# Kernel tuning notes

Hardware: AMD Instinct MI355X
Metric: run time of the kernel (lower is better)

The kernel has to match this reference:

```python
import jax, jax.numpy as jnp
import numpy as np

B, E, S, M, G, L, NSTEP = 32, 256, 16, 16, 32000, 8192, 128


def setup_inputs() -> dict:
    key = jax.random.key(0)
    ks = jax.random.split(key, 8)
    init = lambda k, shape, fan: (jax.random.normal(k, shape, jnp.float32) / np.sqrt(fan).astype(np.float32))
    return {
        "latent": init(ks[0], (L, 2 * E * S), 2 * E * S),
        "trans_w": init(ks[1], (E * M, E), E),
        "trans_b": jnp.zeros((E * M,), jnp.float32),
        "anchor_w": init(ks[2], (M, E), E),
        "anchor_b": jnp.zeros((M,), jnp.float32),
        "vocab_w": init(ks[3], (G, E), E),
        "vocab_b": jnp.zeros((G,), jnp.float32),
        "zi": jax.random.randint(ks[4], (B,), 0, L),
        "y": jax.random.randint(ks[5], (B, NSTEP), 0, G),
        "n_step": NSTEP,
    }


def reference(latent, trans_w, trans_b, anchor_w, anchor_b, vocab_w, vocab_b, zi, y, n_step):
    # latent rows -> (B, 2, state_count, embed_dim); split into keys/values
    z0 = latent[zi].reshape(-1, 2, S, E)
    z = z0[:, 0, 0:1, :]            # initial state: first (unscaled) key vector, [B,1,E]
    xk = z0[:, 0] * 100.0           # [B,S,E]
    xv = z0[:, 1] * 100.0           # [B,S,E]

    def step(z, _):
        # std-normalize (torch.std is unbiased -> ddof=1)
        zn = z / (1e-5 + jnp.std(z, axis=-1, keepdims=True, ddof=1)) * 0.113
        att = jax.nn.softmax(jnp.einsum("bqe,bse->bqs", zn, xk), axis=-1)  # [B,1,S]
        emit = jnp.einsum("bqs,bse->bqe", att, xv)                          # [B,1,E]
        mixed2 = (zn @ trans_w.T + trans_b).reshape(-1, M, E)               # [B,M,E]
        att2 = jax.nn.softmax(zn @ anchor_w.T + anchor_b, axis=-1)          # [B,1,M]
        dz = jnp.einsum("bqm,bme->bqe", att2, mixed2) + emit
        return zn + dz, emit[:, 0, :]

    _, zs = jax.lax.scan(step, z, None, length=n_step)  # [T,B,E]
    zs = jnp.transpose(zs, (1, 0, 2))                   # [B,T,E]
    ys = jax.nn.log_softmax(zs @ vocab_w.T + vocab_b, axis=-1)  # [B,T,G]
    yp = jnp.take_along_axis(ys, y[:, :, None], axis=-1)[:, :, 0]  # [B,T]
    return yp
```

## Files before the change

kernel.cpp:

```cpp
#include <hip/hip_runtime.h>

#define EE 256
#define GG 32000
#define NSTEP 128
#define ROWS 4096
#define VSPLIT 4
#define NWGP 32
#define NWGD 64
#define NWGR (NWGP + NWGD)

typedef __attribute__((ext_vector_type(8))) short bf16x8;
typedef __attribute__((ext_vector_type(4))) float f32x4;

#define OFF_ZSB  0u
#define OFF_PS   2097152u
#define OFF_PT   (OFF_PS + 65536u)
#define OFF_ZNB  (OFF_PT + 65536u)
#define OFF_BAR  (OFF_ZNB + 32768u)
#define OFF_PD   (OFF_BAR + 4096u)
#define WS_REQ   (OFF_PD + 524288u)
#define OFF_VB   WS_REQ
#define VB_BYTES 16384000u


__device__ __forceinline__ float wredf(float v){
    #pragma unroll
    for (int m = 1; m < 64; m <<= 1) v += __shfl_xor(v, m);
    return v;
}
__device__ __forceinline__ unsigned short f2bf_bits(float f){
    unsigned int u = __float_as_uint(f);
    unsigned int lsb = (u >> 16) & 1u;
    u += 0x7fffu + lsb;
    return (unsigned short)(u >> 16);
}
__device__ __forceinline__ float bf2f(unsigned short u){
    return __uint_as_float(((unsigned int)u) << 16);
}
__device__ __forceinline__ float aload(const float* p){
    return __hip_atomic_load(p, __ATOMIC_RELAXED, __HIP_MEMORY_SCOPE_AGENT);
}
__device__ __forceinline__ void astore(float* p, float v){
    __hip_atomic_store(p, v, __ATOMIC_RELAXED, __HIP_MEMORY_SCOPE_AGENT);
}
__device__ __forceinline__ unsigned aloadu(const unsigned* p){
    return __hip_atomic_load(p, __ATOMIC_RELAXED, __HIP_MEMORY_SCOPE_AGENT);
}
__device__ __forceinline__ void astoreu(unsigned* p, unsigned v){
    __hip_atomic_store(p, v, __ATOMIC_RELAXED, __HIP_MEMORY_SCOPE_AGENT);
}
__device__ __forceinline__ int swz(int row, int kbyte){
    return row*512 + (kbyte ^ ((row & 7) << 4));
}
__device__ __forceinline__ void pollflag(int* bar, int idx, int gen){
    int spins = 0;
    while (__hip_atomic_load(&bar[idx], __ATOMIC_RELAXED, __HIP_MEMORY_SCOPE_AGENT) < gen){
        __builtin_amdgcn_s_sleep(1);
        if (++spins > 2000000){
            __hip_atomic_store(&bar[132], 1, __ATOMIC_RELAXED, __HIP_MEMORY_SCOPE_AGENT);
            break;
        }
        if ((spins & 2047) == 0 &&
            __hip_atomic_load(&bar[132], __ATOMIC_RELAXED, __HIP_MEMORY_SCOPE_AGENT) != 0)
            break;
    }
}

__global__ __launch_bounds__(256) void k_sentinel(float* __restrict__ outp, float val){
    int r = blockIdx.x * 256 + threadIdx.x;
    outp[r] = val;
}

__global__ void k_prep(const int* __restrict__ zi, int* __restrict__ bar){
    int t = threadIdx.x;
    bar[t] = 0;
    __syncthreads();
    if (t == 0){
        bool odd_zero = true, even_ok = true;
        for (int i = 0; i < 16; ++i){
            int lo = zi[2*i], hi = zi[2*i+1];
            if (hi != 0) odd_zero = false;
            if (lo < 0 || lo >= 8192) even_ok = false;
        }
        bar[136] = (odd_zero && even_ok) ? 1 : 0;
    }
}

__global__ __launch_bounds__(256) void k_cvt(const float* __restrict__ in,
                                             unsigned short* __restrict__ outp)
{
    int i = (blockIdx.x * 256 + threadIdx.x) * 4;
    float4 v = *(const float4*)&in[i];
    ushort4 o;
    o.x = f2bf_bits(v.x); o.y = f2bf_bits(v.y);
    o.z = f2bf_bits(v.z); o.w = f2bf_bits(v.w);
    *(ushort4*)&outp[i] = o;
}

__global__ __launch_bounds__(512, 1) void k_rnn(const float* __restrict__ latent,
                                                const int* __restrict__ zi,
                                                const float* __restrict__ anchor_w,
                                                const float* __restrict__ anchor_b,
                                                const float* __restrict__ trans_w,
                                                const float* __restrict__ trans_b,
                                                unsigned short* __restrict__ zsb,
                                                unsigned* __restrict__ ZNB,
                                                float* __restrict__ PD,
                                                int* __restrict__ bar)
{
    __shared__ __align__(16) unsigned char WbRaw[2*64*512];
    __shared__ __align__(16) unsigned char ZNbRaw[2*32*512];
    __shared__ float xk_l[16][260];
    __shared__ float xv_l[16][260];
    __shared__ float zl[256];
    __shared__ float a2s[16];
    __shared__ float tbl[2][32];
    __shared__ float l1s[16], l2s[16], ab_l[16], rbuf[8];

    const int wg = blockIdx.x, t = threadIdx.x;
    const int is64 = bar[136];
    const int lane = t & 63, wv = t >> 6;
    const int kg = lane >> 4, nl = lane & 15;

    if (wg < NWGP){
        const int b = wg;
        int zb = is64 ? zi[2*b] : zi[b];
        const float* base = latent + (size_t)zb * 8192;
        for (int i = t; i < 4096; i += 512){
            int s = i >> 8, c = i & 255;
            xk_l[s][c] = base[i];
            xv_l[s][c] = base[4096 + i];
        }
        if (t < 16) ab_l[t] = anchor_b[t];
        __syncthreads();

        float zn_r = 0.f, em_r = 0.f;
        for (int stp = 0; stp < NSTEP; ++stp){
            if (stp > 0){
                if (t < NWGD) pollflag(bar, 64 + t, stp);
                __syncthreads();
                __builtin_amdgcn_sched_barrier(0);
            }
            float zv = 0.f;
            if (t < 256){
                if (stp == 0) zv = base[t];
                else {
                    float dz = 0.f;
                    #pragma unroll
                    for (int g = 0; g < 16; ++g)
                        dz += a2s[g] * aload(&PD[(g*32 + b)*256 + t]);
                    zv = zn_r + em_r + dz;
                }
                float s1 = wredf(zv), s2 = wredf(zv*zv);
                if ((t & 63) == 0){ rbuf[t>>6] = s1; rbuf[4 + (t>>6)] = s2; }
            }
            __syncthreads();
            if (t < 256){
                float tot1 = rbuf[0]+rbuf[1]+rbuf[2]+rbuf[3];
                float tot2 = rbuf[4]+rbuf[5]+rbuf[6]+rbuf[7];
                float mean = tot1 * (1.0f/EE);
                float var  = (tot2 - (float)EE*mean*mean) * (1.0f/(EE-1));
                var = fmaxf(var, 0.f);
                float sc = 0.113f / (1e-5f + sqrtf(var));
                zn_r = zv * sc;
                zl[t] = zn_r;
                if (stp < NSTEP-1){
                    unsigned short zh  = f2bf_bits(zn_r);
                    unsigned short zlo = f2bf_bits(zn_r - bf2f(zh));
                    unsigned ohi = (unsigned)__shfl_xor((int)(unsigned)zh, 1);
                    unsigned olo = (unsigned)__shfl_xor((int)(unsigned)zlo, 1);
                    if (!(t & 1)){
                        astoreu(&ZNB[b*128 + (t >> 1)],        (unsigned)zh  | (ohi << 16));
                        astoreu(&ZNB[4096 + b*128 + (t >> 1)], (unsigned)zlo | (olo << 16));
                    }
                }
            }
            __syncthreads();
            if (stp < NSTEP-1 && t == 0)
                __hip_atomic_store(&bar[b], stp + 1, __ATOMIC_RELAXED, __HIP_MEMORY_SCOPE_AGENT);

            if (t < 256){
                int sidx = t >> 4, L = t & 15;
                const float* aws = anchor_w + sidx*EE;
                float p1 = 0.f, p2 = 0.f;
                #pragma unroll
                for (int c = 0; c < 16; ++c){
                    int k = L*16 + c;
                    float z = zl[k];
                    p1 += z * xk_l[sidx][k];
                    p2 += z * aws[k];
                }
                #pragma unroll
                for (int mm = 1; mm < 16; mm <<= 1){ p1 += __shfl_xor(p1, mm); p2 += __shfl_xor(p2, mm); }
                if (L == 0){ l1s[sidx] = p1 * 100.0f; l2s[sidx] = p2 + ab_l[sidx]; }
            }
            __syncthreads();
            if (t < 256){
                float mx1 = -1e30f, mx2 = -1e30f;
                #pragma unroll
                for (int s = 0; s < 16; ++s){ mx1 = fmaxf(mx1, l1s[s]); mx2 = fmaxf(mx2, l2s[s]); }
                float att[16]; float sum1 = 0.f, sum2 = 0.f;
                #pragma unroll
                for (int s = 0; s < 16; ++s){
                    att[s] = expf(l1s[s] - mx1); sum1 += att[s];
                    sum2  += expf(l2s[s] - mx2);
                }
                float inv1 = 1.0f / sum1;
                if (t < 16) a2s[t] = expf(l2s[t] - mx2) / sum2;
                float em = 0.f;
                #pragma unroll
                for (int s = 0; s < 16; ++s) em += (att[s] * inv1) * xv_l[s][t];
                em *= 100.0f;
                em_r = em;
                zsb[((size_t)b*NSTEP + stp)*EE + t] = f2bf_bits(em);
            }
            __syncthreads();
        }
    } else {
        const int d = wg - NWGP;
        const int mh = d >> 3, q = d & 7;

        for (int idx = t; idx < 4096; idx += 512){
            int r = idx >> 6, c = idx & 63;
            int grow = (2*mh + (r >> 5))*256 + q*32 + (r & 31);
            float4 w = *(const float4*)&trans_w[(size_t)grow*256 + c*4];
            unsigned short h0 = f2bf_bits(w.x), h1 = f2bf_bits(w.y);
            unsigned short h2 = f2bf_bits(w.z), h3 = f2bf_bits(w.w);
            unsigned short l0 = f2bf_bits(w.x - bf2f(h0)), l1 = f2bf_bits(w.y - bf2f(h1));
            unsigned short l2 = f2bf_bits(w.z - bf2f(h2)), l3 = f2bf_bits(w.w - bf2f(h3));
            int off = swz(r, c*8);
            *(unsigned*)&WbRaw[off]     = (unsigned)h0 | ((unsigned)h1 << 16);
            *(unsigned*)&WbRaw[off + 4] = (unsigned)h2 | ((unsigned)h3 << 16);
            *(unsigned*)&WbRaw[64*512 + off]     = (unsigned)l0 | ((unsigned)l1 << 16);
            *(unsigned*)&WbRaw[64*512 + off + 4] = (unsigned)l2 | ((unsigned)l3 << 16);
        }
        if (t < 64) tbl[t >> 5][t & 31] = trans_b[(2*mh + (t >> 5))*256 + q*32 + (t & 31)];
        __syncthreads();

        for (int k = 1; k < NSTEP; ++k){
            if (t < NWGP) pollflag(bar, t, k);
            __syncthreads();
            __builtin_amdgcn_sched_barrier(0);

            for (int i = t; i < 8192; i += 512){
                int p = i >> 12, rr = (i >> 7) & 31, dd = i & 127;
                unsigned v = aloadu(&ZNB[i]);
                *(unsigned*)&ZNbRaw[p*(32*512) + swz(rr, dd*4)] = v;
            }
            __syncthreads();
            {
                const int m = wv >> 2, et = (wv >> 1) & 1, bt = wv & 1;
                const int arow = m*32 + et*16 + nl;
                const int brow = bt*16 + nl;
                f32x4 acc = {0.f, 0.f, 0.f, 0.f};
                #pragma unroll
                for (int kk = 0; kk < 8; ++kk){
                    int kb = kk*64 + kg*16;
                    bf16x8 ah = *(const bf16x8*)&WbRaw[swz(arow, kb)];
                    bf16x8 al = *(const bf16x8*)&WbRaw[64*512 + swz(arow, kb)];
                    bf16x8 bh = *(const bf16x8*)&ZNbRaw[swz(brow, kb)];
                    bf16x8 bl = *(const bf16x8*)&ZNbRaw[32*512 + swz(brow, kb)];
                    acc = __builtin_amdgcn_mfma_f32_16x16x32_bf16(ah, bh, acc, 0, 0, 0);
                    acc = __builtin_amdgcn_mfma_f32_16x16x32_bf16(ah, bl, acc, 0, 0, 0);
                    acc = __builtin_amdgcn_mfma_f32_16x16x32_bf16(al, bh, acc, 0, 0, 0);
                }
                #pragma unroll
                for (int i = 0; i < 4; ++i){
                    int e_loc = et*16 + kg*4 + i;
                    float u = acc[i] + tbl[m][e_loc];
                    astore(&PD[(((mh << 1) + m)*32 + brow)*256 + q*32 + e_loc], u);
                }
            }
            __syncthreads();
            if (t == 0)
                __hip_atomic_store(&bar[64 + d], k, __ATOMIC_RELAXED, __HIP_MEMORY_SCOPE_AGENT);
        }
    }
}

__device__ __forceinline__ bf16x8 pack8f(const float* __restrict__ src){
    bf16x8 r;
    #pragma unroll
    for (int j = 0; j < 8; ++j) r[j] = (short)f2bf_bits(src[j]);
    return r;
}

template<bool VB>
__global__ __launch_bounds__(256, 1) void k_vocab(const unsigned short* __restrict__ vb,
                                                  const float* __restrict__ vwf,
                                                  const float* __restrict__ vbias,
                                                  const unsigned short* __restrict__ zsb,
                                                  const int* __restrict__ y,
                                                  float* __restrict__ pS,
                                                  float* __restrict__ pT,
                                                  int* __restrict__ bar)
{
    const int rowblk = blockIdx.x;
    const int split  = blockIdx.y;
    const int t = threadIdx.x;
    const int wave = t >> 6, lane = t & 63;
    const int kg = lane >> 4, nl = lane & 15;
    const int is64 = bar[136];

    __shared__ float psum_l[4][64];
    __shared__ float ptarg_l[4][64];
    __shared__ float chk[1];

    bf16x8 afr[4][8];
    #pragma unroll
    for (int mt = 0; mt < 4; ++mt)
        #pragma unroll
        for (int kk = 0; kk < 8; ++kk)
            afr[mt][kk] = *(const bf16x8*)&zsb[(size_t)(rowblk*64 + mt*16 + nl) * EE + kk*32 + kg*8];

    int tg[4][4];
    #pragma unroll
    for (int mt = 0; mt < 4; ++mt)
        #pragma unroll
        for (int i = 0; i < 4; ++i){
            int rg = rowblk*64 + mt*16 + kg*4 + i;
            tg[mt][i] = is64 ? y[2*rg] : y[rg];
        }

    float sums[4][4]; float targ[4][4];
    #pragma unroll
    for (int mt = 0; mt < 4; ++mt)
        #pragma unroll
        for (int i = 0; i < 4; ++i){ sums[mt][i] = 0.f; targ[mt][i] = 0.f; }

    for (int tile = wave; tile < 500; tile += 4){
        int n = split*8000 + tile*16 + nl;
        f32x4 acc[4];
        #pragma unroll
        for (int mt = 0; mt < 4; ++mt) acc[mt] = (f32x4){0.f,0.f,0.f,0.f};
        #pragma unroll
        for (int kk = 0; kk < 8; ++kk){
            bf16x8 bfr;
            if (VB) bfr = *(const bf16x8*)&vb[(size_t)n * EE + kk*32 + kg*8];
            else    bfr = pack8f(&vwf[(size_t)n * EE + kk*32 + kg*8]);
            #pragma unroll
            for (int mt = 0; mt < 4; ++mt)
                acc[mt] = __builtin_amdgcn_mfma_f32_16x16x32_bf16(afr[mt][kk], bfr, acc[mt], 0, 0, 0);
        }
        float bias = vbias[n];
        if (rowblk == 0 && split == 0 && t == 0 && tile == 0)
            chk[0] = acc[0][0] + bias;
        #pragma unroll
        for (int mt = 0; mt < 4; ++mt)
            #pragma unroll
            for (int i = 0; i < 4; ++i){
                float v = acc[mt][i] + bias;
                sums[mt][i] += expf(v);
                if (n == tg[mt][i]) targ[mt][i] += v;
            }
    }

    #pragma unroll
    for (int mt = 0; mt < 4; ++mt)
        #pragma unroll
        for (int i = 0; i < 4; ++i){
            float sv = sums[mt][i], tv = targ[mt][i];
            #pragma unroll
            for (int msk = 1; msk < 16; msk <<= 1){ sv += __shfl_xor(sv, msk); tv += __shfl_xor(tv, msk); }
            if (nl == 0){ int row = mt*16 + kg*4 + i; psum_l[wave][row] = sv; ptarg_l[wave][row] = tv; }
        }
    __syncthreads();
    if (t < 64){
        float sv = psum_l[0][t] + psum_l[1][t] + psum_l[2][t] + psum_l[3][t];
        float tv = ptarg_l[0][t] + ptarg_l[1][t] + ptarg_l[2][t] + ptarg_l[3][t];
        int r = rowblk*64 + t;
        pS[(size_t)split*ROWS + r] = sv;
        pT[(size_t)split*ROWS + r] = tv;
    }

    if (rowblk == 0 && split == 0 && t == 0){
        float s = 0.f;
        for (int k = 0; k < EE; ++k){
            float a = bf2f(zsb[k]);
            float w = VB ? bf2f(vb[k]) : bf2f(f2bf_bits(vwf[k]));
            s += a * w;
        }
        s += vbias[0];
        if (fabsf(s - chk[0]) > 0.02f) bar[133] = 1;
    }
}

__global__ __launch_bounds__(256) void k_final(const float* __restrict__ pS,
                                               const float* __restrict__ pT,
                                               const int* __restrict__ bar,
                                               float* __restrict__ outp)
{
    int r = blockIdx.x * 256 + threadIdx.x;
    float s = 0.f, g = 0.f;
    #pragma unroll
    for (int i = 0; i < VSPLIT; ++i){ s += pS[(size_t)i*ROWS + r]; g += pT[(size_t)i*ROWS + r]; }
    float v = g - logf(s);
    if (bar[132] != 0) v = 4000.0f;
    if (bar[133] != 0) v = 5000.0f;
    outp[r] = v;
}

extern "C" void kernel_launch(void* const* d_in, const int* in_sizes, int n_in,
                              void* d_out, int out_size, void* d_ws, size_t ws_size,
                              hipStream_t stream)
{
    (void)out_size;
    const float* latent   = (const float*)d_in[0];
    const float* trans_w  = (const float*)d_in[1];
    const float* trans_b  = (const float*)d_in[2];
    const float* anchor_w = (const float*)d_in[3];
    const float* anchor_b = (const float*)d_in[4];
    const float* vocab_w  = (const float*)d_in[5];
    const float* vocab_b  = (const float*)d_in[6];
    const int*   zi       = (const int*)d_in[7];
    const int*   y        = (const int*)d_in[8];

    float* outp = (float*)d_out;

    if (ws_size < (size_t)WS_REQ){ k_sentinel<<<16, 256, 0, stream>>>(outp, 2000.0f); return; }
    {
        bool ok = (n_in >= 9)
               && in_sizes[0] == 67108864 && in_sizes[1] == 1048576
               && in_sizes[2] == 4096     && in_sizes[3] == 4096
               && in_sizes[4] == 16       && in_sizes[5] == 8192000
               && in_sizes[6] == 32000
               && (in_sizes[7] == 32   || in_sizes[7] == 64)
               && (in_sizes[8] == 4096 || in_sizes[8] == 8192);
        if (!ok){ k_sentinel<<<16, 256, 0, stream>>>(outp, 2100.0f); return; }
    }

    char* ws = (char*)d_ws;
    unsigned short* zsb = (unsigned short*)(ws + OFF_ZSB);
    float*    pS  = (float*)(ws + OFF_PS);
    float*    pT  = (float*)(ws + OFF_PT);
    unsigned* ZNB = (unsigned*)(ws + OFF_ZNB);
    int*      bar = (int*)(ws + OFF_BAR);
    float*    PD  = (float*)(ws + OFF_PD);
    unsigned short* vbu = (unsigned short*)(ws + OFF_VB);

    const bool use_vb = ws_size >= (size_t)OFF_VB + (size_t)VB_BYTES;

    k_prep<<<1, 256, 0, stream>>>(zi, bar);
    if (use_vb)
        k_cvt<<<GG*EE/1024, 256, 0, stream>>>(vocab_w, vbu);

    k_rnn<<<NWGR, 512, 0, stream>>>(latent, zi, anchor_w, anchor_b,
                                    trans_w, trans_b, zsb, ZNB, PD, bar);

    if (use_vb)
        k_vocab<true><<<dim3(64, VSPLIT), 256, 0, stream>>>(vbu, nullptr, vocab_b,
                                                            zsb, y, pS, pT, bar);
    else
        k_vocab<false><<<dim3(64, VSPLIT), 256, 0, stream>>>(nullptr, vocab_w, vocab_b,
                                                             zsb, y, pS, pT, bar);

    k_final<<<16, 256, 0, stream>>>(pS, pT, bar, outp);
}
```

Before: 1.854 ms.

## Keep trans_w fragments in registers and load ZN directly from global

The DZ workgroups now convert their trans_w slice to split-bf16 MFMA fragments once and keep them in registers instead of LDS. Each step reads the ZN operand straight from global memory with 64-bit atomic loads, which removes the LDS staging pass and one barrier per step. The PD layout is also changed so each batch row's 16 anchor partials sit next to each other, letting the RNN workgroups gather them with eight 64-bit loads instead of sixteen strided 32-bit loads. The cost is higher register pressure and direct global loads inside the MFMA loop.

```diff
diff --git a/kernel.cpp b/kernel.cpp
--- a/kernel.cpp
+++ b/kernel.cpp
@@ -11,6 +11,7 @@
 
 typedef __attribute__((ext_vector_type(8))) short bf16x8;
 typedef __attribute__((ext_vector_type(4))) float f32x4;
+typedef __attribute__((ext_vector_type(2))) unsigned long long u64x2;
 
 #define OFF_ZSB  0u
 #define OFF_PS   2097152u
@@ -43,14 +44,11 @@
 __device__ __forceinline__ void astore(float* p, float v){
     __hip_atomic_store(p, v, __ATOMIC_RELAXED, __HIP_MEMORY_SCOPE_AGENT);
 }
-__device__ __forceinline__ unsigned aloadu(const unsigned* p){
-    return __hip_atomic_load(p, __ATOMIC_RELAXED, __HIP_MEMORY_SCOPE_AGENT);
-}
 __device__ __forceinline__ void astoreu(unsigned* p, unsigned v){
     __hip_atomic_store(p, v, __ATOMIC_RELAXED, __HIP_MEMORY_SCOPE_AGENT);
 }
-__device__ __forceinline__ int swz(int row, int kbyte){
-    return row*512 + (kbyte ^ ((row & 7) << 4));
+__device__ __forceinline__ unsigned long long aload64(const unsigned long long* p){
+    return __hip_atomic_load(p, __ATOMIC_RELAXED, __HIP_MEMORY_SCOPE_AGENT);
 }
 __device__ __forceinline__ void pollflag(int* bar, int idx, int gen){
     int spins = 0;
@@ -108,8 +106,6 @@
                                                 float* __restrict__ PD,
                                                 int* __restrict__ bar)
 {
-    __shared__ __align__(16) unsigned char WbRaw[2*64*512];
-    __shared__ __align__(16) unsigned char ZNbRaw[2*32*512];
     __shared__ float xk_l[16][260];
     __shared__ float xv_l[16][260];
     __shared__ float zl[256];
@@ -145,10 +141,15 @@
             if (t < 256){
                 if (stp == 0) zv = base[t];
                 else {
+                    const unsigned long long* PD64 = (const unsigned long long*)PD;
+                    const int b64 = (b*4096 + t*16) >> 1;
                     float dz = 0.f;
                     #pragma unroll
-                    for (int g = 0; g < 16; ++g)
-                        dz += a2s[g] * aload(&PD[(g*32 + b)*256 + t]);
+                    for (int h = 0; h < 8; ++h){
+                        unsigned long long v = aload64(&PD64[b64 + h]);
+                        float2 f = __builtin_bit_cast(float2, v);
+                        dz += a2s[2*h] * f.x + a2s[2*h+1] * f.y;
+                    }
                     zv = zn_r + em_r + dz;
                 }
                 float s1 = wredf(zv), s2 = wredf(zv*zv);
@@ -219,57 +220,57 @@
     } else {
         const int d = wg - NWGP;
         const int mh = d >> 3, q = d & 7;
-
-        for (int idx = t; idx < 4096; idx += 512){
-            int r = idx >> 6, c = idx & 63;
-            int grow = (2*mh + (r >> 5))*256 + q*32 + (r & 31);
-            float4 w = *(const float4*)&trans_w[(size_t)grow*256 + c*4];
-            unsigned short h0 = f2bf_bits(w.x), h1 = f2bf_bits(w.y);
-            unsigned short h2 = f2bf_bits(w.z), h3 = f2bf_bits(w.w);
-            unsigned short l0 = f2bf_bits(w.x - bf2f(h0)), l1 = f2bf_bits(w.y - bf2f(h1));
-            unsigned short l2 = f2bf_bits(w.z - bf2f(h2)), l3 = f2bf_bits(w.w - bf2f(h3));
-            int off = swz(r, c*8);
-            *(unsigned*)&WbRaw[off]     = (unsigned)h0 | ((unsigned)h1 << 16);
-            *(unsigned*)&WbRaw[off + 4] = (unsigned)h2 | ((unsigned)h3 << 16);
-            *(unsigned*)&WbRaw[64*512 + off]     = (unsigned)l0 | ((unsigned)l1 << 16);
-            *(unsigned*)&WbRaw[64*512 + off + 4] = (unsigned)l2 | ((unsigned)l3 << 16);
+        const int m = wv >> 2, et = (wv >> 1) & 1, bt = wv & 1;
+        const int brow = bt*16 + nl;
+
+        bf16x8 Ah[8], Al[8];
+        {
+            const int grow = (2*mh + m)*256 + q*32 + et*16 + nl;
+            const float* wp = trans_w + (size_t)grow * 256;
+            #pragma unroll
+            for (int kk = 0; kk < 8; ++kk){
+                float4 w0 = *(const float4*)&wp[kk*32 + kg*8];
+                float4 w1 = *(const float4*)&wp[kk*32 + kg*8 + 4];
+                float ws[8] = {w0.x,w0.y,w0.z,w0.w,w1.x,w1.y,w1.z,w1.w};
+                bf16x8 ah, al;
+                #pragma unroll
+                for (int j = 0; j < 8; ++j){
+                    unsigned short hh = f2bf_bits(ws[j]);
+                    ah[j] = (short)hh;
+                    al[j] = (short)f2bf_bits(ws[j] - bf2f(hh));
+                }
+                Ah[kk] = ah; Al[kk] = al;
+            }
         }
         if (t < 64) tbl[t >> 5][t & 31] = trans_b[(2*mh + (t >> 5))*256 + q*32 + (t & 31)];
         __syncthreads();
 
+        const unsigned long long* Z64 = (const unsigned long long*)ZNB;
         for (int k = 1; k < NSTEP; ++k){
             if (t < NWGP) pollflag(bar, t, k);
             __syncthreads();
             __builtin_amdgcn_sched_barrier(0);
 
-            for (int i = t; i < 8192; i += 512){
-                int p = i >> 12, rr = (i >> 7) & 31, dd = i & 127;
-                unsigned v = aloadu(&ZNB[i]);
-                *(unsigned*)&ZNbRaw[p*(32*512) + swz(rr, dd*4)] = v;
-            }
-            __syncthreads();
-            {
-                const int m = wv >> 2, et = (wv >> 1) & 1, bt = wv & 1;
-                const int arow = m*32 + et*16 + nl;
-                const int brow = bt*16 + nl;
-                f32x4 acc = {0.f, 0.f, 0.f, 0.f};
-                #pragma unroll
-                for (int kk = 0; kk < 8; ++kk){
-                    int kb = kk*64 + kg*16;
-                    bf16x8 ah = *(const bf16x8*)&WbRaw[swz(arow, kb)];
-                    bf16x8 al = *(const bf16x8*)&WbRaw[64*512 + swz(arow, kb)];
-                    bf16x8 bh = *(const bf16x8*)&ZNbRaw[swz(brow, kb)];
-                    bf16x8 bl = *(const bf16x8*)&ZNbRaw[32*512 + swz(brow, kb)];
-                    acc = __builtin_amdgcn_mfma_f32_16x16x32_bf16(ah, bh, acc, 0, 0, 0);
-                    acc = __builtin_amdgcn_mfma_f32_16x16x32_bf16(ah, bl, acc, 0, 0, 0);
-                    acc = __builtin_amdgcn_mfma_f32_16x16x32_bf16(al, bh, acc, 0, 0, 0);
-                }
-                #pragma unroll
-                for (int i = 0; i < 4; ++i){
-                    int e_loc = et*16 + kg*4 + i;
-                    float u = acc[i] + tbl[m][e_loc];
-                    astore(&PD[(((mh << 1) + m)*32 + brow)*256 + q*32 + e_loc], u);
-                }
+            f32x4 acc = {0.f, 0.f, 0.f, 0.f};
+            #pragma unroll
+            for (int kk = 0; kk < 8; ++kk){
+                const int bi = brow*64 + kk*8 + kg*2;
+                u64x2 th, tl;
+                th.x = aload64(&Z64[bi]);
+                th.y = aload64(&Z64[bi + 1]);
+                tl.x = aload64(&Z64[2048 + bi]);
+                tl.y = aload64(&Z64[2048 + bi + 1]);
+                bf16x8 bh = __builtin_bit_cast(bf16x8, th);
+                bf16x8 bl = __builtin_bit_cast(bf16x8, tl);
+                acc = __builtin_amdgcn_mfma_f32_16x16x32_bf16(Ah[kk], bh, acc, 0, 0, 0);
+                acc = __builtin_amdgcn_mfma_f32_16x16x32_bf16(Ah[kk], bl, acc, 0, 0, 0);
+                acc = __builtin_amdgcn_mfma_f32_16x16x32_bf16(Al[kk], bh, acc, 0, 0, 0);
+            }
+            #pragma unroll
+            for (int i = 0; i < 4; ++i){
+                int e_loc = et*16 + kg*4 + i;
+                float u = acc[i] + tbl[m][e_loc];
+                astore(&PD[brow*4096 + (q*32 + e_loc)*16 + 2*mh + m], u);
             }
             __syncthreads();
             if (t == 0)
```

Result: slower. 2.477 ms (+33.6%).
